# Kernel optimization log

Measured on AMD Instinct MI355X. Metric: run time of the kernel, lower is better.

## Reference

```python
import jax, jax.numpy as jnp
import numpy as np

B, CIN, MID, OUT = 4096, 64, 256, 256
K = CIN * 25  # flattened 5x5 patch per channel
EPS = 1e-5


def _masks():
    # [3, 25] binary masks over the 5x5 kernel for the 3 branch families
    circle = np.zeros((5, 5), np.float32); circle[1:4, 1:4] = 1.0
    corner = np.zeros((5, 5), np.float32)
    for (i, j) in [(0, 0), (0, 4), (4, 0), (4, 4), (2, 2)]:
        corner[i, j] = 1.0
    horse = np.zeros((5, 5), np.float32)
    for (i, j) in [(0, 1), (0, 3), (1, 0), (1, 4), (3, 0), (3, 4), (4, 1), (4, 3), (2, 2)]:
        horse[i, j] = 1.0
    return jnp.asarray(np.stack([circle, corner, horse]).reshape(3, 25))


def mish(x):
    return x * jnp.tanh(jax.nn.softplus(x))


def setup_inputs() -> dict:
    key = jax.random.key(0)
    ks = jax.random.split(key, 12)
    x = jax.random.normal(ks[0], (B, CIN, 7, 7), jnp.float32)
    W5 = jax.random.normal(ks[1], (27, MID, K), jnp.float32) * 0.05
    b5 = jax.random.normal(ks[2], (27, MID), jnp.float32) * 0.05
    gamma = jnp.ones((27, MID), jnp.float32)
    beta = jnp.zeros((27, MID), jnp.float32)
    run_mean = jax.random.normal(ks[3], (27, MID), jnp.float32) * 0.05
    run_var = jax.random.uniform(ks[4], (27, MID), jnp.float32, 0.5, 1.5)
    W1 = jax.random.normal(ks[5], (27, MID, MID), jnp.float32) * 0.05
    b1 = jax.random.normal(ks[6], (27, MID), jnp.float32) * 0.05
    W2 = jax.random.normal(ks[7], (27, OUT, MID), jnp.float32) * 0.05
    b2 = jax.random.normal(ks[8], (27, OUT), jnp.float32) * 0.05
    return {"x": x, "W5": W5, "b5": b5, "gamma": gamma, "beta": beta,
            "run_mean": run_mean, "run_var": run_var,
            "W1": W1, "b1": b1, "W2": W2, "b2": b2}


def reference(x, W5, b5, gamma, beta, run_mean, run_var, W1, b1, W2, b2):
    masks = _masks()  # [3,25]
    # 9 patches of 5x5: [9, B, CIN*25]
    patches = jnp.stack([x[:, :, k:k + 5, v:v + 5]
                         for k in range(3) for v in range(3)])
    patches = patches.reshape(9, B, K)
    # mask kernels per branch family and group weights as [3,9,MID,K]
    mask_k = jnp.repeat(masks, 9, axis=0)          # [27,25]
    mask_k = jnp.tile(mask_k, (1, CIN))[:, None, :]  # [27,1,CIN*25]
    W5m = (W5 * mask_k).reshape(3, 9, MID, K)
    # masked 5x5 conv on 5x5 patch -> 1x1 == dot product: [3,9,B,MID]
    z = jnp.einsum('pbk,gpmk->gpbm', patches, W5m) + b5.reshape(3, 9, 1, MID)
    # BatchNorm (inference, running stats) + Mish
    inv = jax.lax.rsqrt(run_var.reshape(3, 9, 1, MID) + EPS)
    h = mish((z - run_mean.reshape(3, 9, 1, MID)) * inv
             * gamma.reshape(3, 9, 1, MID) + beta.reshape(3, 9, 1, MID))
    # 1x1 conv + Mish, then final 1x1 conv
    h = mish(jnp.einsum('gpbm,gpnm->gpbn', h, W1.reshape(3, 9, MID, MID))
             + b1.reshape(3, 9, 1, MID))
    o = jnp.einsum('gpbm,gpom->gpbo', h, W2.reshape(3, 9, OUT, MID)) \
        + b2.reshape(3, 9, 1, OUT)                 # [3,9,B,OUT]
    copy_features = o[0].sum(0)                    # sum of 9 circle branches
    jump_features = o[1].sum(0) + o[2].sum(0)      # sum of 18 corner+horse
    # output is 1x1 spatially, so flatten(2).sum(2) is identity on [B,OUT]
    return copy_features * jump_features
```

## Files before the change

kernel.cpp:

```cpp
#include <hip/hip_runtime.h>

typedef __bf16 bf16x8 __attribute__((ext_vector_type(8)));
typedef float f32x4 __attribute__((ext_vector_type(4)));

__constant__ int SL_I[3][9] = {{1,1,1,2,2,2,3,3,3},{0,0,2,4,4,0,0,0,0},{0,0,1,1,2,3,3,4,4}};
__constant__ int SL_J[3][9] = {{1,2,3,1,2,3,1,2,3},{0,4,2,0,4,0,0,0,0},{1,3,0,4,2,0,4,1,3}};
__constant__ int SL_S[3][9] = {{6,7,8,11,12,13,16,17,18},{0,4,12,20,24,0,0,0,0},{1,3,5,9,12,15,19,21,23}};

#define GLDS16(gsrc, ldst)                                                        \
  __builtin_amdgcn_global_load_lds(                                               \
      (const __attribute__((address_space(1))) unsigned int*)(gsrc),              \
      (__attribute__((address_space(3))) unsigned int*)(ldst), 16, 0, 0)

static __device__ __forceinline__ unsigned short f2b(float f) {
  return __builtin_bit_cast(unsigned short, (__bf16)f);
}
static __device__ __forceinline__ float b2f(unsigned short u) {
  unsigned int b = ((unsigned int)u) << 16;
  return __builtin_bit_cast(float, b);
}
static __device__ __forceinline__ float mish_f(float x) {
  float u = __expf(x);
  float w = u * (u + 2.0f);
  float r = x * w * __builtin_amdgcn_rcpf(w + 2.0f);
  return (x > 20.0f) ? x : r;
}
static __device__ __forceinline__ int swz8(int c, int r) {
  return ((((c >> 3) ^ (r & 7)) << 3) | (c & 7));
}

__global__ __launch_bounds__(256) void prep_x_k(const float* __restrict__ X,
                                                unsigned short* __restrict__ Xb) {
  __shared__ float tile[3136];
  const int b = blockIdx.x;
  const float* xp = X + (size_t)b * 3136;
  for (int i = threadIdx.x; i < 3136; i += 256) tile[i] = xp[i];
  __syncthreads();
  for (int i = threadIdx.x; i < 3136; i += 256) {
    int s = i >> 6, c = i & 63;
    Xb[(size_t)s * 262144 + (size_t)b * 64 + swz8(c, b)] = f2b(tile[c * 49 + s]);
  }
}

__global__ __launch_bounds__(256) void prep_w5_k(const float* __restrict__ W5,
                                                 unsigned short* __restrict__ W5c) {
  int idx = blockIdx.x * 256 + threadIdx.x;
  if (idx >= 27 * 256 * 9 * 64) return;
  int c = idx & 63;
  int t2 = idx >> 6;
  int u = t2 % 9;
  int gm = t2 / 9;
  int m = gm & 255;
  int g = (gm >> 8) / 9;
  int nm = (g == 1) ? 5 : 9;
  if (u >= nm) return;
  int c_src = swz8(c, m);
  W5c[idx] = f2b(W5[(size_t)gm * 1600 + c_src * 25 + SL_S[g][u]]);
}

__global__ __launch_bounds__(256) void prep_w12_k(const float* __restrict__ W1, const float* __restrict__ W2,
                                                  unsigned short* __restrict__ W1b, unsigned short* __restrict__ W2b) {
  int idx = blockIdx.x * 256 + threadIdx.x;
  if (idx < 27 * 256 * 256) {
    int n = (idx >> 8) & 255;
    int c = idx & 63;
    int src = (idx & ~63) | swz8(c, n);
    W1b[idx] = f2b(W1[src]);
    W2b[idx] = f2b(W2[src]);
  }
}

__global__ __launch_bounds__(256) void prep_bn_k(const float* __restrict__ b5, const float* __restrict__ gamma,
                                                 const float* __restrict__ beta, const float* __restrict__ rmean,
                                                 const float* __restrict__ rvar,
                                                 float* __restrict__ bn_a, float* __restrict__ bn_c) {
  int i = blockIdx.x * 256 + threadIdx.x;
  if (i < 27 * 256) {
    float a = gamma[i] * rsqrtf(rvar[i] + 1e-5f);
    bn_a[i] = a;
    bn_c[i] = (b5[i] - rmean[i]) * a + beta[i];
  }
}

__global__ __launch_bounds__(512) void gemm1_k(const unsigned short* __restrict__ Xb,
                                               const unsigned short* __restrict__ W5c,
                                               const float* __restrict__ bn_a, const float* __restrict__ bn_c,
                                               unsigned short* __restrict__ H) {
  __shared__ unsigned short smem[32768];
  const int t = threadIdx.x;
  const int lane = t & 63;
  const int w = t >> 6;
  const int wm = w >> 2, wn = w & 3;
  const int l15 = lane & 15, l4 = lane >> 4;
  const int sw = l15 & 7;
  const int m0 = blockIdx.x * 128, n0 = blockIdx.y * 128;
  const int gp = blockIdx.z;
  const int g = gp / 9, p = gp - g * 9;
  const int pk = p / 3, pv = p - pk * 3;
  const int nm = (g == 1) ? 5 : 9;

  const f32x4 zero = {0.f, 0.f, 0.f, 0.f};
  f32x4 acc[4][2];
#pragma unroll
  for (int i = 0; i < 4; ++i)
#pragma unroll
    for (int j = 0; j < 2; ++j) acc[i][j] = zero;

  auto STAGE = [&](int pbuf, int u) {
    const int s = (pk + SL_I[g][u]) * 7 + (pv + SL_J[g][u]);
    const unsigned short* srcA = Xb + (size_t)s * 262144 + (size_t)m0 * 64;
    unsigned short* dA = smem + pbuf * 16384;
    unsigned short* dB = dA + 8192;
#pragma unroll
    for (int it = 0; it < 2; ++it) {
      int idx = it * 512 + t;
      GLDS16(srcA + idx * 8, dA + idx * 8);
    }
#pragma unroll
    for (int it = 0; it < 2; ++it) {
      int idx = it * 512 + t;
      int row = idx >> 3, ch = idx & 7;
      GLDS16(W5c + (size_t)(gp * 256 + n0 + row) * 576 + u * 64 + ch * 8, dB + idx * 8);
    }
  };

  STAGE(0, 0);
  __syncthreads();
  int cur = 0;
  for (int u = 0; u < nm; ++u) {
    if (u + 1 < nm) STAGE(cur ^ 1, u + 1);
    const unsigned short* lA = smem + cur * 16384;
    const unsigned short* lB = lA + 8192;
#pragma unroll
    for (int kk = 0; kk < 2; ++kk) {
      bf16x8 af[4], bfr[2];
#pragma unroll
      for (int f4 = 0; f4 < 4; ++f4)
        af[f4] = *reinterpret_cast<const bf16x8*>(lA + (wm * 64 + f4 * 16 + l15) * 64 + (((kk * 4 + l4) ^ sw) << 3));
#pragma unroll
      for (int f2 = 0; f2 < 2; ++f2)
        bfr[f2] = *reinterpret_cast<const bf16x8*>(lB + (wn * 32 + f2 * 16 + l15) * 64 + (((kk * 4 + l4) ^ sw) << 3));
#pragma unroll
      for (int i = 0; i < 4; ++i)
#pragma unroll
        for (int j = 0; j < 2; ++j)
          acc[i][j] = __builtin_amdgcn_mfma_f32_16x16x32_bf16(af[i], bfr[j], acc[i][j], 0, 0, 0);
    }
    __syncthreads();
    cur ^= 1;
  }
#pragma unroll
  for (int j = 0; j < 2; ++j) {
    const int col = wn * 32 + j * 16 + l15;
    const float a  = bn_a[gp * 256 + n0 + col];
    const float cc = bn_c[gp * 256 + n0 + col];
#pragma unroll
    for (int i = 0; i < 4; ++i) {
      const int r0 = wm * 64 + i * 16 + l4 * 4;
#pragma unroll
      for (int e = 0; e < 4; ++e) {
        const int r = r0 + e;
        float z = acc[i][j][e] * a + cc;
        smem[r * 128 + (col ^ ((r & 7) << 3))] = f2b(mish_f(z));
      }
    }
  }
  __syncthreads();
  {
    unsigned short* Hg = H + (size_t)gp * 1048576;
#pragma unroll
    for (int it = 0; it < 4; ++it) {
      int idx = it * 512 + t;
      int row = idx >> 4, seg = idx & 15;
      int c8 = (seg * 8) ^ ((row & 7) << 3);
      uint4 v = *(const uint4*)(smem + row * 128 + c8);
      int colout = n0 + (seg >> 3) * 64 + (((seg & 7) ^ (row & 7)) << 3);
      *(uint4*)(Hg + (size_t)(m0 + row) * 256 + colout) = v;
    }
  }
}

__global__ __launch_bounds__(512) void gemm23_k(const unsigned short* __restrict__ A, const unsigned short* __restrict__ Bw,
                                                const float* __restrict__ bias, unsigned short* __restrict__ Out,
                                                int act, int swz_out) {
  __shared__ unsigned short smem[32768];
  const int t = threadIdx.x;
  const int lane = t & 63;
  const int w = t >> 6;
  const int wm = w >> 2, wn = w & 3;
  const int l15 = lane & 15, l4 = lane >> 4;
  const int sw = l15 & 7;
  const int m0 = blockIdx.x * 128, n0 = blockIdx.y * 128;
  const int gp = blockIdx.z;

  const f32x4 zero = {0.f, 0.f, 0.f, 0.f};
  f32x4 acc[4][2];
#pragma unroll
  for (int i = 0; i < 4; ++i)
#pragma unroll
    for (int j = 0; j < 2; ++j) acc[i][j] = zero;

  auto STAGE = [&](int pbuf, int kt) {
    unsigned short* dA = smem + pbuf * 16384;
    unsigned short* dB = dA + 8192;
#pragma unroll
    for (int it = 0; it < 2; ++it) {
      int idx = it * 512 + t;
      int row = idx >> 3, ch = idx & 7;
      GLDS16(A + (size_t)(gp * 4096 + m0 + row) * 256 + kt * 64 + ch * 8, dA + idx * 8);
      GLDS16(Bw + (size_t)(gp * 256 + n0 + row) * 256 + kt * 64 + ch * 8, dB + idx * 8);
    }
  };

  STAGE(0, 0);
  __syncthreads();
  int cur = 0;
  for (int kt = 0; kt < 4; ++kt) {
    if (kt + 1 < 4) STAGE(cur ^ 1, kt + 1);
    const unsigned short* lA = smem + cur * 16384;
    const unsigned short* lB = lA + 8192;
#pragma unroll
    for (int kk = 0; kk < 2; ++kk) {
      bf16x8 af[4], bfr[2];
#pragma unroll
      for (int f4 = 0; f4 < 4; ++f4)
        af[f4] = *reinterpret_cast<const bf16x8*>(lA + (wm * 64 + f4 * 16 + l15) * 64 + (((kk * 4 + l4) ^ sw) << 3));
#pragma unroll
      for (int f2 = 0; f2 < 2; ++f2)
        bfr[f2] = *reinterpret_cast<const bf16x8*>(lB + (wn * 32 + f2 * 16 + l15) * 64 + (((kk * 4 + l4) ^ sw) << 3));
#pragma unroll
      for (int i = 0; i < 4; ++i)
#pragma unroll
        for (int j = 0; j < 2; ++j)
          acc[i][j] = __builtin_amdgcn_mfma_f32_16x16x32_bf16(af[i], bfr[j], acc[i][j], 0, 0, 0);
    }
    __syncthreads();
    cur ^= 1;
  }
#pragma unroll
  for (int j = 0; j < 2; ++j) {
    const int col = wn * 32 + j * 16 + l15;
    const float bi = bias[gp * 256 + n0 + col];
#pragma unroll
    for (int i = 0; i < 4; ++i) {
      const int r0 = wm * 64 + i * 16 + l4 * 4;
#pragma unroll
      for (int e = 0; e < 4; ++e) {
        const int r = r0 + e;
        float z = acc[i][j][e] + bi;
        if (act) z = mish_f(z);
        smem[r * 128 + (col ^ ((r & 7) << 3))] = f2b(z);
      }
    }
  }
  __syncthreads();
  {
    unsigned short* Og = Out + (size_t)gp * 1048576;
#pragma unroll
    for (int it = 0; it < 4; ++it) {
      int idx = it * 512 + t;
      int row = idx >> 4, seg = idx & 15;
      int c8 = (seg * 8) ^ ((row & 7) << 3);
      uint4 v = *(const uint4*)(smem + row * 128 + c8);
      int colout = swz_out ? (seg >> 3) * 64 + (((seg & 7) ^ (row & 7)) << 3) : seg * 8;
      *(uint4*)(Og + (size_t)(m0 + row) * 256 + n0 + colout) = v;
    }
  }
}

__global__ __launch_bounds__(256) void final_k(const unsigned short* __restrict__ O, float* __restrict__ out) {
  const size_t base = ((size_t)blockIdx.x * 256 + threadIdx.x) * 8;
  float cs[8], js[8];
#pragma unroll
  for (int e = 0; e < 8; ++e) { cs[e] = 0.f; js[e] = 0.f; }
#pragma unroll
  for (int gp = 0; gp < 27; ++gp) {
    uint4 v = *(const uint4*)(O + (size_t)gp * 1048576 + base);
    const unsigned short* pv = (const unsigned short*)&v;
    if (gp < 9) {
#pragma unroll
      for (int e = 0; e < 8; ++e) cs[e] += b2f(pv[e]);
    } else {
#pragma unroll
      for (int e = 0; e < 8; ++e) js[e] += b2f(pv[e]);
    }
  }
  float4 o0 = {cs[0] * js[0], cs[1] * js[1], cs[2] * js[2], cs[3] * js[3]};
  float4 o1 = {cs[4] * js[4], cs[5] * js[5], cs[6] * js[6], cs[7] * js[7]};
  *(float4*)(out + base) = o0;
  *(float4*)(out + base + 4) = o1;
}

extern "C" void kernel_launch(void* const* d_in, const int* in_sizes, int n_in,
                              void* d_out, int out_size, void* d_ws, size_t ws_size,
                              hipStream_t stream) {
  const float* X     = (const float*)d_in[0];
  const float* W5    = (const float*)d_in[1];
  const float* b5    = (const float*)d_in[2];
  const float* gamma = (const float*)d_in[3];
  const float* beta  = (const float*)d_in[4];
  const float* rmean = (const float*)d_in[5];
  const float* rvar  = (const float*)d_in[6];
  const float* W1    = (const float*)d_in[7];
  const float* b1    = (const float*)d_in[8];
  const float* W2    = (const float*)d_in[9];
  const float* b2    = (const float*)d_in[10];
  float* out = (float*)d_out;
  char* ws = (char*)d_ws;

  unsigned short* W5c  = (unsigned short*)(ws);
  unsigned short* W1b  = (unsigned short*)(ws + 7962624);
  unsigned short* W2b  = (unsigned short*)(ws + 11501568);
  float*          bn_a = (float*)(ws + 15040512);
  float*          bn_c = (float*)(ws + 15068160);
  unsigned short* Xb   = (unsigned short*)(ws + 15095808);
  unsigned short* Hbuf = (unsigned short*)(ws + 40785920);
  unsigned short* H1b  = (unsigned short*)(ws + 97409024);
  unsigned short* Obuf = Hbuf;

  prep_x_k<<<4096, 256, 0, stream>>>(X, Xb);
  prep_w5_k<<<15552, 256, 0, stream>>>(W5, W5c);
  prep_w12_k<<<6912, 256, 0, stream>>>(W1, W2, W1b, W2b);
  prep_bn_k<<<27, 256, 0, stream>>>(b5, gamma, beta, rmean, rvar, bn_a, bn_c);

  gemm1_k<<<dim3(32, 2, 27), 512, 0, stream>>>(Xb, W5c, bn_a, bn_c, Hbuf);
  gemm23_k<<<dim3(32, 2, 27), 512, 0, stream>>>(Hbuf, W1b, b1, H1b, 1, 1);
  gemm23_k<<<dim3(32, 2, 27), 512, 0, stream>>>(H1b, W2b, b2, Obuf, 0, 0);
  final_k<<<512, 256, 0, stream>>>(Obuf, out);
}
```

Baseline: 170.9 us.

## Fuse the two 1x1-conv GEMMs into one kernel keeping H1 in LDS

Merges the W1 GEMM (with Mish) and the W2 GEMM into a single kernel. Each block computes a full 128x256 tile, keeps the intermediate activation in shared memory and feeds it straight into the second GEMM, so the H1 global write and read-back and one launch go away. In exchange it uses 128KB of dynamic LDS, which lowers occupancy to one block per CU and halves the block count. The B-operand staging is now single-buffered with extra barriers, which may expose load latency.

```diff
diff --git a/kernel.cpp b/kernel.cpp
--- a/kernel.cpp
+++ b/kernel.cpp
@@ -27,6 +27,9 @@
 }
 static __device__ __forceinline__ int swz8(int c, int r) {
   return ((((c >> 3) ^ (r & 7)) << 3) | (c & 7));
+}
+static __device__ __forceinline__ int swoff(int c, int r) {
+  return (c & ~63) | ((c & 63) ^ ((r & 7) << 3));
 }
 
 __global__ __launch_bounds__(256) void prep_x_k(const float* __restrict__ X,
@@ -180,90 +183,142 @@
   }
 }
 
-__global__ __launch_bounds__(512) void gemm23_k(const unsigned short* __restrict__ A, const unsigned short* __restrict__ Bw,
-                                                const float* __restrict__ bias, unsigned short* __restrict__ Out,
-                                                int act, int swz_out) {
-  __shared__ unsigned short smem[32768];
+__global__ __launch_bounds__(512) void gemm23f_k(const unsigned short* __restrict__ Hb,
+                                                 const unsigned short* __restrict__ W1b,
+                                                 const unsigned short* __restrict__ W2b,
+                                                 const float* __restrict__ b1, const float* __restrict__ b2,
+                                                 unsigned short* __restrict__ Obuf) {
+  extern __shared__ unsigned short smem[];
+  unsigned short* h1  = smem;
+  unsigned short* stA = smem + 32768;
+  unsigned short* stB = smem + 49152;
   const int t = threadIdx.x;
   const int lane = t & 63;
   const int w = t >> 6;
   const int wm = w >> 2, wn = w & 3;
   const int l15 = lane & 15, l4 = lane >> 4;
   const int sw = l15 & 7;
-  const int m0 = blockIdx.x * 128, n0 = blockIdx.y * 128;
-  const int gp = blockIdx.z;
+  const int m0 = blockIdx.x * 128;
+  const int gp = blockIdx.y;
 
   const f32x4 zero = {0.f, 0.f, 0.f, 0.f};
-  f32x4 acc[4][2];
+  f32x4 acc[4][4];
 #pragma unroll
   for (int i = 0; i < 4; ++i)
 #pragma unroll
-    for (int j = 0; j < 2; ++j) acc[i][j] = zero;
-
-  auto STAGE = [&](int pbuf, int kt) {
-    unsigned short* dA = smem + pbuf * 16384;
-    unsigned short* dB = dA + 8192;
+    for (int j = 0; j < 4; ++j) acc[i][j] = zero;
+
+  auto STAGE_A = [&](int pbuf, int kt) {
+    unsigned short* dA = stA + pbuf * 8192;
 #pragma unroll
     for (int it = 0; it < 2; ++it) {
       int idx = it * 512 + t;
-      int row = idx >> 3, ch = idx & 7;
-      GLDS16(A + (size_t)(gp * 4096 + m0 + row) * 256 + kt * 64 + ch * 8, dA + idx * 8);
-      GLDS16(Bw + (size_t)(gp * 256 + n0 + row) * 256 + kt * 64 + ch * 8, dB + idx * 8);
+      GLDS16(Hb + (size_t)(gp * 4096 + m0 + (idx >> 3)) * 256 + kt * 64 + (idx & 7) * 8, dA + idx * 8);
     }
   };
-
-  STAGE(0, 0);
+  auto STAGE_B = [&](const unsigned short* W, int kt) {
+#pragma unroll
+    for (int it = 0; it < 4; ++it) {
+      int idx = it * 512 + t;
+      GLDS16(W + (size_t)(gp * 256 + (idx >> 3)) * 256 + kt * 64 + (idx & 7) * 8, stB + idx * 8);
+    }
+  };
+
+  STAGE_A(0, 0);
+  STAGE_B(W1b, 0);
   __syncthreads();
   int cur = 0;
   for (int kt = 0; kt < 4; ++kt) {
-    if (kt + 1 < 4) STAGE(cur ^ 1, kt + 1);
-    const unsigned short* lA = smem + cur * 16384;
-    const unsigned short* lB = lA + 8192;
+    if (kt < 3) STAGE_A(cur ^ 1, kt + 1);
+    const unsigned short* lA = stA + cur * 8192;
 #pragma unroll
     for (int kk = 0; kk < 2; ++kk) {
-      bf16x8 af[4], bfr[2];
+      bf16x8 af[4], bfr[4];
 #pragma unroll
       for (int f4 = 0; f4 < 4; ++f4)
         af[f4] = *reinterpret_cast<const bf16x8*>(lA + (wm * 64 + f4 * 16 + l15) * 64 + (((kk * 4 + l4) ^ sw) << 3));
 #pragma unroll
-      for (int f2 = 0; f2 < 2; ++f2)
-        bfr[f2] = *reinterpret_cast<const bf16x8*>(lB + (wn * 32 + f2 * 16 + l15) * 64 + (((kk * 4 + l4) ^ sw) << 3));
+      for (int f4 = 0; f4 < 4; ++f4)
+        bfr[f4] = *reinterpret_cast<const bf16x8*>(stB + (wn * 64 + f4 * 16 + l15) * 64 + (((kk * 4 + l4) ^ sw) << 3));
 #pragma unroll
       for (int i = 0; i < 4; ++i)
 #pragma unroll
-        for (int j = 0; j < 2; ++j)
+        for (int j = 0; j < 4; ++j)
           acc[i][j] = __builtin_amdgcn_mfma_f32_16x16x32_bf16(af[i], bfr[j], acc[i][j], 0, 0, 0);
     }
     __syncthreads();
+    if (kt < 3) {
+      STAGE_B(W1b, kt + 1);
+      __syncthreads();
+    }
     cur ^= 1;
   }
 #pragma unroll
-  for (int j = 0; j < 2; ++j) {
-    const int col = wn * 32 + j * 16 + l15;
-    const float bi = bias[gp * 256 + n0 + col];
+  for (int j = 0; j < 4; ++j) {
+    const int c = wn * 64 + j * 16 + l15;
+    const float bi = b1[gp * 256 + c];
 #pragma unroll
     for (int i = 0; i < 4; ++i) {
       const int r0 = wm * 64 + i * 16 + l4 * 4;
 #pragma unroll
       for (int e = 0; e < 4; ++e) {
         const int r = r0 + e;
-        float z = acc[i][j][e] + bi;
-        if (act) z = mish_f(z);
-        smem[r * 128 + (col ^ ((r & 7) << 3))] = f2b(z);
+        h1[r * 256 + swoff(c, r)] = f2b(mish_f(acc[i][j][e] + bi));
       }
     }
   }
   __syncthreads();
+
+#pragma unroll
+  for (int i = 0; i < 4; ++i)
+#pragma unroll
+    for (int j = 0; j < 4; ++j) acc[i][j] = zero;
+  for (int kt = 0; kt < 4; ++kt) {
+    STAGE_B(W2b, kt);
+    __syncthreads();
+#pragma unroll
+    for (int kk = 0; kk < 2; ++kk) {
+      bf16x8 af[4], bfr[4];
+#pragma unroll
+      for (int f4 = 0; f4 < 4; ++f4)
+        af[f4] = *reinterpret_cast<const bf16x8*>(
+            h1 + (wm * 64 + f4 * 16 + l15) * 256 + kt * 64 + (((kk * 4 + l4) ^ sw) << 3));
+#pragma unroll
+      for (int f4 = 0; f4 < 4; ++f4)
+        bfr[f4] = *reinterpret_cast<const bf16x8*>(stB + (wn * 64 + f4 * 16 + l15) * 64 + (((kk * 4 + l4) ^ sw) << 3));
+#pragma unroll
+      for (int i = 0; i < 4; ++i)
+#pragma unroll
+        for (int j = 0; j < 4; ++j)
+          acc[i][j] = __builtin_amdgcn_mfma_f32_16x16x32_bf16(af[i], bfr[j], acc[i][j], 0, 0, 0);
+    }
+    __syncthreads();
+  }
+  unsigned short* tr = stA;
+#pragma unroll
+  for (int j = 0; j < 4; ++j) {
+    const int c = wn * 64 + j * 16 + l15;
+    const float bi = b2[gp * 256 + c];
+#pragma unroll
+    for (int i = 0; i < 4; ++i) {
+      const int r0 = wm * 64 + i * 16 + l4 * 4;
+#pragma unroll
+      for (int e = 0; e < 4; ++e) {
+        const int r = r0 + e;
+        tr[r * 256 + swoff(c, r)] = f2b(acc[i][j][e] + bi);
+      }
+    }
+  }
+  __syncthreads();
   {
-    unsigned short* Og = Out + (size_t)gp * 1048576;
-#pragma unroll
-    for (int it = 0; it < 4; ++it) {
-      int idx = it * 512 + t;
-      int row = idx >> 4, seg = idx & 15;
-      int c8 = (seg * 8) ^ ((row & 7) << 3);
-      uint4 v = *(const uint4*)(smem + row * 128 + c8);
-      int colout = swz_out ? (seg >> 3) * 64 + (((seg & 7) ^ (row & 7)) << 3) : seg * 8;
-      *(uint4*)(Og + (size_t)(m0 + row) * 256 + n0 + colout) = v;
+    unsigned short* Og = Obuf + (size_t)gp * 1048576;
+#pragma unroll
+    for (int it = 0; it < 8; ++it) {
+      int idx = it * 512 + t;
+      int row = idx >> 5, seg = idx & 31;
+      int c8 = swoff(seg * 8, row);
+      uint4 v = *(const uint4*)(tr + row * 256 + c8);
+      *(uint4*)(Og + (size_t)(m0 + row) * 256 + seg * 8) = v;
     }
   }
 }
@@ -315,8 +370,10 @@
   float*          bn_c = (float*)(ws + 15068160);
   unsigned short* Xb   = (unsigned short*)(ws + 15095808);
   unsigned short* Hbuf = (unsigned short*)(ws + 40785920);
-  unsigned short* H1b  = (unsigned short*)(ws + 97409024);
-  unsigned short* Obuf = Hbuf;
+  unsigned short* Obuf = (unsigned short*)(ws + 97409024);
+
+  (void)hipFuncSetAttribute(reinterpret_cast<const void*>(gemm23f_k),
+                            hipFuncAttributeMaxDynamicSharedMemorySize, 131072);
 
   prep_x_k<<<4096, 256, 0, stream>>>(X, Xb);
   prep_w5_k<<<15552, 256, 0, stream>>>(W5, W5c);
@@ -324,7 +381,6 @@
   prep_bn_k<<<27, 256, 0, stream>>>(b5, gamma, beta, rmean, rvar, bn_a, bn_c);
 
   gemm1_k<<<dim3(32, 2, 27), 512, 0, stream>>>(Xb, W5c, bn_a, bn_c, Hbuf);
-  gemm23_k<<<dim3(32, 2, 27), 512, 0, stream>>>(Hbuf, W1b, b1, H1b, 1, 1);
-  gemm23_k<<<dim3(32, 2, 27), 512, 0, stream>>>(H1b, W2b, b2, Obuf, 0, 0);
+  gemm23f_k<<<dim3(32, 27), 512, 131072, stream>>>(Hbuf, W1b, W2b, b1, b2, Obuf);
   final_k<<<512, 256, 0, stream>>>(Obuf, out);
 }
```

Measured after the change: 174.7 us. 2.2% more time.
